# Optimization experiments

Measured on AMD Instinct MI355X. Metric: run time of the kernel, lower is better.

The kernel has to match this reference:

```python
import jax, jax.numpy as jnp
import numpy as np

HEADS = 16
LN_EPS = 1e-5


def setup_inputs() -> dict:
    key = jax.random.key(0)
    k0, k1, k2 = jax.random.split(key, 3)
    B, NE, D = 8, 2048, 1024
    qk_scale = np.sqrt(1.0 / D) * np.sqrt(2.0 / (D + 2 * D))  # xavier_normal gain sqrt(qk_w/D)
    v_scale = np.sqrt(0.01 / D) * np.sqrt(2.0 / (D + D))      # xavier_normal gain sqrt(v_w/D)
    return {
        "inp": jax.random.normal(k0, (B, NE, D), dtype=jnp.float32),
        "gamma": jnp.ones((D,), dtype=jnp.float32),
        "beta": jnp.zeros((D,), dtype=jnp.float32),
        "W_qk": jax.random.normal(k1, (D, 2 * D), dtype=jnp.float32) * qk_scale,
        "b_qk": jnp.zeros((2 * D,), dtype=jnp.float32),
        "W_v": jax.random.normal(k2, (D, D), dtype=jnp.float32) * v_scale,
        "b_v": jnp.zeros((D,), dtype=jnp.float32),
    }


def reference(inp, gamma, beta, W_qk, b_qk, W_v, b_v):
    B, NE, D = inp.shape
    hd = D // HEADS
    # LayerNorm over last dim
    mu = jnp.mean(inp, axis=-1, keepdims=True)
    var = jnp.mean(jnp.square(inp - mu), axis=-1, keepdims=True)
    x = (inp - mu) * jax.lax.rsqrt(var + LN_EPS) * gamma + beta
    # fused qk projection; note interleaved q/k layout in last axis of the view
    qk = (jnp.einsum("bnd,de->bne", x, W_qk) + b_qk).reshape(B, NE, HEADS, hd, 2)
    q = qk[..., 0]  # [B, NE, H, hd]
    k = qk[..., 1]
    v = (jnp.einsum("bnd,de->bne", x, W_v) + b_v).reshape(B, NE, HEADS, hd)
    q = jnp.transpose(q, (0, 2, 1, 3))  # [B, H, NE, hd]
    k = jnp.transpose(k, (0, 2, 3, 1))  # [B, H, hd, NE]
    v = jnp.transpose(v, (0, 2, 1, 3))  # [B, H, NE, hd]
    return (q, k, v)
```

## Files before the change

kernel.cpp:

```cpp
#include <hip/hip_runtime.h>
#include <hip/hip_bf16.h>

#define D_DIM 1024
#define M_TOT 16384
#define N_TOT 3072
#define NQK   2048
#define QKV_SZ 16777216

typedef __attribute__((ext_vector_type(8))) __bf16 bf16x8;
typedef __attribute__((ext_vector_type(4))) float floatx4;

__device__ __forceinline__ unsigned short f2bf(float f) {
  unsigned int u = __float_as_uint(f);
  u += 0x7FFFu + ((u >> 16) & 1u);
  return (unsigned short)(u >> 16);
}

__device__ __forceinline__ void gl2lds16(const void* g, void* l) {
  __builtin_amdgcn_global_load_lds(
      (const __attribute__((address_space(1))) void*)g,
      (__attribute__((address_space(3))) void*)l, 16, 0, 0);
}

__global__ __launch_bounds__(256) void ln_kernel(
    const float* __restrict__ inp, const float* __restrict__ gamma,
    const float* __restrict__ beta, unsigned short* __restrict__ X) {
  const int row = blockIdx.x;
  const int t = threadIdx.x;
  const float* rp = inp + (size_t)row * D_DIM;
  float4 v = *(const float4*)(rp + t * 4);
  float s  = v.x + v.y + v.z + v.w;
  float s2 = v.x * v.x + v.y * v.y + v.z * v.z + v.w * v.w;
#pragma unroll
  for (int o = 1; o < 64; o <<= 1) {
    s  += __shfl_xor(s, o);
    s2 += __shfl_xor(s2, o);
  }
  __shared__ float ws[8];
  const int w = t >> 6, l = t & 63;
  if (l == 0) { ws[w] = s; ws[4 + w] = s2; }
  __syncthreads();
  s  = ws[0] + ws[1] + ws[2] + ws[3];
  s2 = ws[4] + ws[5] + ws[6] + ws[7];
  const float mu = s * (1.0f / D_DIM);
  const float var = s2 * (1.0f / D_DIM) - mu * mu;
  const float rstd = rsqrtf(var + 1e-5f);
  float4 g = *(const float4*)(gamma + t * 4);
  float4 b = *(const float4*)(beta + t * 4);
  ushort4 o;
  o.x = f2bf((v.x - mu) * rstd * g.x + b.x);
  o.y = f2bf((v.y - mu) * rstd * g.y + b.y);
  o.z = f2bf((v.z - mu) * rstd * g.z + b.z);
  o.w = f2bf((v.w - mu) * rstd * g.w + b.w);
  *(ushort4*)(X + (size_t)row * D_DIM + t * 4) = o;
}

__global__ __launch_bounds__(256) void wt_kernel(
    const float* __restrict__ Wqk, const float* __restrict__ Wv,
    unsigned short* __restrict__ Wt) {
  __shared__ float tile[64][65];
  const int n0 = blockIdx.x * 64;
  const int k0 = blockIdx.y * 64;
  const float* src;
  int ldn, nc0;
  if (n0 < NQK) { src = Wqk; ldn = NQK; nc0 = n0; }
  else          { src = Wv;  ldn = D_DIM; nc0 = n0 - NQK; }
  const int t = threadIdx.x;
  const int r = t >> 4;
  const int c4 = (t & 15) << 2;
#pragma unroll
  for (int p = 0; p < 4; ++p) {
    int kk = p * 16 + r;
    float4 vv = *(const float4*)(src + (size_t)(k0 + kk) * ldn + nc0 + c4);
    tile[kk][c4 + 0] = vv.x;
    tile[kk][c4 + 1] = vv.y;
    tile[kk][c4 + 2] = vv.z;
    tile[kk][c4 + 3] = vv.w;
  }
  __syncthreads();
#pragma unroll
  for (int p = 0; p < 4; ++p) {
    int nn = p * 16 + r;
    ushort4 o;
    o.x = f2bf(tile[c4 + 0][nn]);
    o.y = f2bf(tile[c4 + 1][nn]);
    o.z = f2bf(tile[c4 + 2][nn]);
    o.w = f2bf(tile[c4 + 3][nn]);
    *(ushort4*)(Wt + (size_t)(n0 + nn) * D_DIM + k0 + c4) = o;
  }
}

__global__ __launch_bounds__(256) void gemm_kernel(
    const unsigned short* __restrict__ X,
    const unsigned short* __restrict__ Wt,
    const float* __restrict__ bqk, const float* __restrict__ bv,
    float* __restrict__ out) {
  __shared__ __align__(16) unsigned short As[128 * 64];
  __shared__ __align__(16) unsigned short Bs[128 * 64];

  const int bm = blockIdx.x / 24;
  const int bn = blockIdx.x % 24;
  const int m0 = bm * 128;
  const int n0 = bn * 128;
  const int tid = threadIdx.x;
  const int w = tid >> 6, l = tid & 63;
  const int wm = w >> 1, wn = w & 1;
  const int lr = l & 15;
  const int lg = l >> 4;

  const int srow = w * 8 + (l >> 3);
  const int scol = (l & 7) * 8;
  const unsigned short* gA = X  + (size_t)(m0 + srow) * D_DIM + scol;
  const unsigned short* gB = Wt + (size_t)(n0 + srow) * D_DIM + scol;
  char* lA = (char*)As + w * 1024;
  char* lB = (char*)Bs + w * 1024;

  floatx4 acc[4][4];
#pragma unroll
  for (int i = 0; i < 4; ++i)
#pragma unroll
    for (int j = 0; j < 4; ++j) acc[i][j] = (floatx4){0.f, 0.f, 0.f, 0.f};

  for (int kt = 0; kt < D_DIM / 64; ++kt) {
    const int ko = kt * 64;
#pragma unroll
    for (int p = 0; p < 4; ++p) {
      gl2lds16(gA + (size_t)(p * 32) * D_DIM + ko, lA + p * 4096);
      gl2lds16(gB + (size_t)(p * 32) * D_DIM + ko, lB + p * 4096);
    }
    __syncthreads();
#pragma unroll
    for (int ks = 0; ks < 2; ++ks) {
      bf16x8 af[4], bf[4];
#pragma unroll
      for (int mi = 0; mi < 4; ++mi)
        af[mi] = *(const bf16x8*)(As + (wm * 64 + mi * 16 + lr) * 64 + ks * 32 + lg * 8);
#pragma unroll
      for (int ni = 0; ni < 4; ++ni)
        bf[ni] = *(const bf16x8*)(Bs + (wn * 64 + ni * 16 + lr) * 64 + ks * 32 + lg * 8);
#pragma unroll
      for (int mi = 0; mi < 4; ++mi)
#pragma unroll
        for (int ni = 0; ni < 4; ++ni)
          acc[mi][ni] = __builtin_amdgcn_mfma_f32_16x16x32_bf16(af[mi], bf[ni], acc[mi][ni], 0, 0, 0);
    }
    __syncthreads();
  }

  const size_t OQ = 0, OK = QKV_SZ, OV = 2 * (size_t)QKV_SZ;
  const int mb = m0 + wm * 64;
  const int bb = mb >> 11;
#pragma unroll
  for (int ni = 0; ni < 4; ++ni) {
    const int col = wn * 64 + ni * 16 + lr;
    const int ng = n0 + col;
#pragma unroll
    for (int mi = 0; mi < 4; ++mi) {
      const int mrow = mb + mi * 16 + lg * 4;
      const int ne = mrow & 2047;
      floatx4 a = acc[mi][ni];
      if (ng < NQK) {
        const float bias = bqk[ng];
        const int h = ng >> 7;
        const int d = (ng & 127) >> 1;
        if ((ng & 1) == 0) {
          float* p = out + OQ + (((size_t)(bb * 16 + h) * 2048 + ne) * 64 + d);
          p[0]   = a[0] + bias;
          p[64]  = a[1] + bias;
          p[128] = a[2] + bias;
          p[192] = a[3] + bias;
        } else {
          float* p = out + OK + ((size_t)(bb * 16 + h) * 64 + d) * 2048 + ne;
          float4 kv = make_float4(a[0] + bias, a[1] + bias, a[2] + bias, a[3] + bias);
          *(float4*)p = kv;
        }
      } else {
        const int nn = ng - NQK;
        const float bias = bv[nn];
        const int h = nn >> 6;
        const int d = nn & 63;
        float* p = out + OV + (((size_t)(bb * 16 + h) * 2048 + ne) * 64 + d);
        p[0]   = a[0] + bias;
        p[64]  = a[1] + bias;
        p[128] = a[2] + bias;
        p[192] = a[3] + bias;
      }
    }
  }
}

extern "C" void kernel_launch(void* const* d_in, const int* in_sizes, int n_in,
                              void* d_out, int out_size, void* d_ws, size_t ws_size,
                              hipStream_t stream) {
  const float* inp   = (const float*)d_in[0];
  const float* gamma = (const float*)d_in[1];
  const float* beta  = (const float*)d_in[2];
  const float* Wqk   = (const float*)d_in[3];
  const float* bqk   = (const float*)d_in[4];
  const float* Wv    = (const float*)d_in[5];
  const float* bv    = (const float*)d_in[6];
  float* out = (float*)d_out;

  unsigned short* X  = (unsigned short*)d_ws;
  unsigned short* Wt = X + (size_t)M_TOT * D_DIM;

  ln_kernel<<<M_TOT, 256, 0, stream>>>(inp, gamma, beta, X);
  wt_kernel<<<dim3(N_TOT / 64, D_DIM / 64), 256, 0, stream>>>(Wqk, Wv, Wt);
  gemm_kernel<<<(M_TOT / 128) * (N_TOT / 128), 256, 0, stream>>>(X, Wt, bqk, bv, out);
}
```

Baseline: 441.9 us.

## Double-buffer GEMM K-loop and stage epilogue through LDS for coalesced stores

The GEMM main loop now double-buffers A/B tiles in a 64KB shared buffer, issuing the next tile's global-to-LDS loads before computing the current one. This removes one barrier per iteration and hides load latency. The epilogue also writes accumulators plus bias into an LDS tile in two passes and then emits float4 stores for the Q, K-transposed and V layouts, replacing the scattered scalar stores. The larger shared allocation may reduce occupancy, and the two-pass epilogue adds extra barriers.

```diff
diff --git a/kernel.cpp b/kernel.cpp
--- a/kernel.cpp
+++ b/kernel.cpp
@@ -95,8 +95,7 @@
     const unsigned short* __restrict__ Wt,
     const float* __restrict__ bqk, const float* __restrict__ bv,
     float* __restrict__ out) {
-  __shared__ __align__(16) unsigned short As[128 * 64];
-  __shared__ __align__(16) unsigned short Bs[128 * 64];
+  __shared__ __align__(16) unsigned char smem[65536];
 
   const int bm = blockIdx.x / 24;
   const int bn = blockIdx.x % 24;
@@ -112,8 +111,7 @@
   const int scol = (l & 7) * 8;
   const unsigned short* gA = X  + (size_t)(m0 + srow) * D_DIM + scol;
   const unsigned short* gB = Wt + (size_t)(n0 + srow) * D_DIM + scol;
-  char* lA = (char*)As + w * 1024;
-  char* lB = (char*)Bs + w * 1024;
+  const int lbase = w * 1024;
 
   floatx4 acc[4][4];
 #pragma unroll
@@ -121,72 +119,117 @@
 #pragma unroll
     for (int j = 0; j < 4; ++j) acc[i][j] = (floatx4){0.f, 0.f, 0.f, 0.f};
 
-  for (int kt = 0; kt < D_DIM / 64; ++kt) {
-    const int ko = kt * 64;
-#pragma unroll
-    for (int p = 0; p < 4; ++p) {
-      gl2lds16(gA + (size_t)(p * 32) * D_DIM + ko, lA + p * 4096);
-      gl2lds16(gB + (size_t)(p * 32) * D_DIM + ko, lB + p * 4096);
+#define STAGE(buf, kt)                                                        \
+  {                                                                           \
+    const int ko_ = (kt) * 64;                                                \
+    unsigned char* la_ = smem + (buf) * 16384 + lbase;                        \
+    unsigned char* lb_ = smem + 32768 + (buf) * 16384 + lbase;                \
+    _Pragma("unroll")                                                         \
+    for (int p = 0; p < 4; ++p) {                                             \
+      gl2lds16(gA + (size_t)(p * 32) * D_DIM + ko_, la_ + p * 4096);          \
+      gl2lds16(gB + (size_t)(p * 32) * D_DIM + ko_, lb_ + p * 4096);          \
+    }                                                                         \
+  }
+
+#define COMPUTE(buf)                                                          \
+  {                                                                           \
+    const unsigned short* As_ = (const unsigned short*)(smem + (buf) * 16384);\
+    const unsigned short* Bs_ = (const unsigned short*)(smem + 32768 + (buf) * 16384); \
+    _Pragma("unroll")                                                         \
+    for (int ks = 0; ks < 2; ++ks) {                                          \
+      bf16x8 af[4], bf[4];                                                    \
+      _Pragma("unroll")                                                       \
+      for (int mi = 0; mi < 4; ++mi)                                          \
+        af[mi] = *(const bf16x8*)(As_ + (wm * 64 + mi * 16 + lr) * 64 + ks * 32 + lg * 8); \
+      _Pragma("unroll")                                                       \
+      for (int ni = 0; ni < 4; ++ni)                                          \
+        bf[ni] = *(const bf16x8*)(Bs_ + (wn * 64 + ni * 16 + lr) * 64 + ks * 32 + lg * 8); \
+      _Pragma("unroll")                                                       \
+      for (int mi = 0; mi < 4; ++mi)                                          \
+        _Pragma("unroll")                                                     \
+        for (int ni = 0; ni < 4; ++ni)                                        \
+          acc[mi][ni] = __builtin_amdgcn_mfma_f32_16x16x32_bf16(af[mi], bf[ni], acc[mi][ni], 0, 0, 0); \
+    }                                                                         \
+  }
+
+  STAGE(0, 0);
+  __syncthreads();
+  int cur = 0;
+#pragma unroll 1
+  for (int kt = 0; kt < 15; ++kt) {
+    STAGE(cur ^ 1, kt + 1);
+    COMPUTE(cur);
+    __syncthreads();
+    cur ^= 1;
+  }
+  COMPUTE(cur);
+
+  const size_t OQ = 0, OK = QKV_SZ, OV = 2 * (size_t)QKV_SZ;
+  const int bb = m0 >> 11;
+  const int mloc = m0 & 2047;
+  float* Cf = (float*)smem;
+
+#pragma unroll 1
+  for (int pass = 0; pass < 2; ++pass) {
+    __syncthreads();
+    if (wn == pass) {
+#pragma unroll
+      for (int ni = 0; ni < 4; ++ni) {
+        const int cl = ni * 16 + lr;
+        const int ng = n0 + pass * 64 + cl;
+        const float bias = (ng < NQK) ? bqk[ng] : bv[ng - NQK];
+#pragma unroll
+        for (int mi = 0; mi < 4; ++mi) {
+          const int r0 = wm * 64 + mi * 16 + lg * 4;
+#pragma unroll
+          for (int j = 0; j < 4; ++j)
+            Cf[(r0 + j) * 65 + cl] = acc[mi][ni][j] + bias;
+        }
+      }
     }
     __syncthreads();
-#pragma unroll
-    for (int ks = 0; ks < 2; ++ks) {
-      bf16x8 af[4], bf[4];
-#pragma unroll
-      for (int mi = 0; mi < 4; ++mi)
-        af[mi] = *(const bf16x8*)(As + (wm * 64 + mi * 16 + lr) * 64 + ks * 32 + lg * 8);
-#pragma unroll
-      for (int ni = 0; ni < 4; ++ni)
-        bf[ni] = *(const bf16x8*)(Bs + (wn * 64 + ni * 16 + lr) * 64 + ks * 32 + lg * 8);
-#pragma unroll
-      for (int mi = 0; mi < 4; ++mi)
-#pragma unroll
-        for (int ni = 0; ni < 4; ++ni)
-          acc[mi][ni] = __builtin_amdgcn_mfma_f32_16x16x32_bf16(af[mi], bf[ni], acc[mi][ni], 0, 0, 0);
+    if (n0 < NQK) {
+      const int h = n0 >> 7;
+      {
+        const int row = tid >> 1, doff = (tid & 1) * 16;
+        const int d0 = pass * 32 + doff;
+        float* qp = out + OQ + (((size_t)(bb * 16 + h) * 2048 + mloc + row) * 64) + d0;
+        float vbuf[16];
+#pragma unroll
+        for (int i = 0; i < 16; ++i)
+          vbuf[i] = Cf[row * 65 + 2 * (doff + i)];
+#pragma unroll
+        for (int i4 = 0; i4 < 4; ++i4)
+          *(float4*)(qp + i4 * 4) = make_float4(vbuf[i4*4], vbuf[i4*4+1], vbuf[i4*4+2], vbuf[i4*4+3]);
+      }
+      {
+        const int dl = tid >> 3;
+        const int neo = (tid & 7) * 16;
+        const int d = pass * 32 + dl;
+        float* kp = out + OK + (((size_t)(bb * 16 + h) * 64 + d) * 2048) + mloc + neo;
+        float vbuf[16];
+#pragma unroll
+        for (int i = 0; i < 16; ++i)
+          vbuf[i] = Cf[(neo + i) * 65 + 2 * dl + 1];
+#pragma unroll
+        for (int i4 = 0; i4 < 4; ++i4)
+          *(float4*)(kp + i4 * 4) = make_float4(vbuf[i4*4], vbuf[i4*4+1], vbuf[i4*4+2], vbuf[i4*4+3]);
+      }
+    } else {
+      const int vbase = (n0 - NQK) + pass * 64;
+      const int h = vbase >> 6;
+      const int row = tid >> 1, off = (tid & 1) * 32;
+      float* vp = out + OV + (((size_t)(bb * 16 + h) * 2048 + mloc + row) * 64) + off;
+#pragma unroll
+      for (int i4 = 0; i4 < 8; ++i4) {
+        float4 t4 = make_float4(Cf[row * 65 + off + i4*4],     Cf[row * 65 + off + i4*4 + 1],
+                                Cf[row * 65 + off + i4*4 + 2], Cf[row * 65 + off + i4*4 + 3]);
+        *(float4*)(vp + i4 * 4) = t4;
+      }
     }
-    __syncthreads();
-  }
-
-  const size_t OQ = 0, OK = QKV_SZ, OV = 2 * (size_t)QKV_SZ;
-  const int mb = m0 + wm * 64;
-  const int bb = mb >> 11;
-#pragma unroll
-  for (int ni = 0; ni < 4; ++ni) {
-    const int col = wn * 64 + ni * 16 + lr;
-    const int ng = n0 + col;
-#pragma unroll
-    for (int mi = 0; mi < 4; ++mi) {
-      const int mrow = mb + mi * 16 + lg * 4;
-      const int ne = mrow & 2047;
-      floatx4 a = acc[mi][ni];
-      if (ng < NQK) {
-        const float bias = bqk[ng];
-        const int h = ng >> 7;
-        const int d = (ng & 127) >> 1;
-        if ((ng & 1) == 0) {
-          float* p = out + OQ + (((size_t)(bb * 16 + h) * 2048 + ne) * 64 + d);
-          p[0]   = a[0] + bias;
-          p[64]  = a[1] + bias;
-          p[128] = a[2] + bias;
-          p[192] = a[3] + bias;
-        } else {
-          float* p = out + OK + ((size_t)(bb * 16 + h) * 64 + d) * 2048 + ne;
-          float4 kv = make_float4(a[0] + bias, a[1] + bias, a[2] + bias, a[3] + bias);
-          *(float4*)p = kv;
-        }
-      } else {
-        const int nn = ng - NQK;
-        const float bias = bv[nn];
-        const int h = nn >> 6;
-        const int d = nn & 63;
-        float* p = out + OV + (((size_t)(bb * 16 + h) * 2048 + ne) * 64 + d);
-        p[0]   = a[0] + bias;
-        p[64]  = a[1] + bias;
-        p[128] = a[2] + bias;
-        p[192] = a[3] + bias;
-      }
-    }
-  }
+  }
+#undef STAGE
+#undef COMPUTE
 }
 
 extern "C" void kernel_launch(void* const* d_in, const int* in_sizes, int n_in,
```

Result: faster. 414.2 us (-6.3%).
